# Kernel tuning notes

Measured on AMD Instinct MI355X. Metric: run time of the kernel, lower is better.

## Reference

```python
import jax, jax.numpy as jnp
import numpy as np

V, D, H, L, B, T = 32000, 1024, 1024, 4, 32, 128
PAD_ID = 0


def setup_inputs() -> dict:
    key = jax.random.key(0)
    ks = jax.random.split(key, 12)
    s = lambda fan: 1.0 / np.sqrt(fan)
    dec_input = jax.random.randint(ks[0], (B, T), 0, V)
    h0 = jax.random.normal(ks[1], (L, B, H), jnp.float32)
    c0 = jax.random.normal(ks[2], (L, B, H), jnp.float32)
    emb = jax.random.normal(ks[3], (V, D), jnp.float32) * 0.02
    emb = emb.at[PAD_ID].set(0.0)
    # all layers have input size H (layer0 input = embedding_dim = H)
    W_ih = jax.random.uniform(ks[4], (L, 4 * H, H), jnp.float32, -s(H), s(H))
    W_hh = jax.random.uniform(ks[5], (L, 4 * H, H), jnp.float32, -s(H), s(H))
    b_ih = jax.random.uniform(ks[6], (L, 4 * H), jnp.float32, -s(H), s(H))
    b_hh = jax.random.uniform(ks[7], (L, 4 * H), jnp.float32, -s(H), s(H))
    cls_W = jax.random.uniform(ks[8], (V, H), jnp.float32, -s(H), s(H))
    cls_b = jax.random.uniform(ks[9], (V,), jnp.float32, -s(H), s(H))
    return {"dec_input": dec_input, "h0": h0, "c0": c0, "emb": emb,
            "W_ih": W_ih, "W_hh": W_hh, "b_ih": b_ih, "b_hh": b_hh,
            "cls_W": cls_W, "cls_b": cls_b}


def _lstm_stack_step(carry, x_t, W_ih, W_hh, b_ih, b_hh):
    # carry: (h [L,B,H], c [L,B,H]); x_t: [B,H]
    h, c = carry
    inp = x_t
    hs, cs = [], []
    n_layers = W_ih.shape[0]
    for l in range(n_layers):
        gates = inp @ W_ih[l].T + h[l] @ W_hh[l].T + b_ih[l] + b_hh[l]
        i_g, f_g, g_g, o_g = jnp.split(gates, 4, axis=-1)
        c_new = jax.nn.sigmoid(f_g) * c[l] + jax.nn.sigmoid(i_g) * jnp.tanh(g_g)
        h_new = jax.nn.sigmoid(o_g) * jnp.tanh(c_new)
        inp = h_new + inp  # residual connection (dropout p=0)
        hs.append(h_new)
        cs.append(c_new)
    return (jnp.stack(hs, 0), jnp.stack(cs, 0)), inp


def reference(dec_input, h0, c0, emb, W_ih, W_hh, b_ih, b_hh, cls_W, cls_b):
    embedded = emb[dec_input]                 # [B,T,D]
    xs = jnp.swapaxes(embedded, 0, 1)         # [T,B,D]

    def step(carry, x_t):
        return _lstm_stack_step(carry, x_t, W_ih, W_hh, b_ih, b_hh)

    (hT, cT), outs = jax.lax.scan(step, (h0, c0), xs)  # outs: [T,B,H]
    outputs = jnp.swapaxes(outs, 0, 1)         # [B,T,H]
    logits = outputs @ cls_W.T + cls_b         # [B,T,V]
    return logits, (hT, cT)
```

## Files before the change

kernel.cpp:

```cpp
#include <hip/hip_runtime.h>
#include <stdint.h>

#define LAYERS 4
#define BATCH  32
#define SEQT   128
#define HID    1024
#define VOCAB  32000

typedef __attribute__((ext_vector_type(8))) short short8;
typedef __attribute__((ext_vector_type(8))) __bf16 bf16x8;
typedef __attribute__((ext_vector_type(4))) float floatx4;

#define CLS_OFF  0ul
#define X_OFF    65536000ul
#define RES_OFF  73924608ul
#define HB_OFF   107479040ul
#define CF_OFF   108003328ul
#define SYNC_OFF 108527616ul

#define LOGITS_N 131072000ul

__device__ __forceinline__ unsigned short f2bf(float f) {
  union { float f; unsigned u; } v; v.f = f;
  unsigned r = v.u + 0x7FFF + ((v.u >> 16) & 1);
  return (unsigned short)(r >> 16);
}
__device__ __forceinline__ float bf2f(unsigned short b) {
  union { unsigned u; float f; } v; v.u = ((unsigned)b) << 16;
  return v.f;
}
__device__ __forceinline__ floatx4 mfma16(short8 a, short8 b, floatx4 c) {
  return __builtin_amdgcn_mfma_f32_16x16x32_bf16(
      __builtin_bit_cast(bf16x8, a), __builtin_bit_cast(bf16x8, b), c, 0, 0, 0);
}
__device__ __forceinline__ short8 cvt8(float4 a, float4 b) {
  short8 r;
  r[0] = (short)f2bf(a.x); r[1] = (short)f2bf(a.y);
  r[2] = (short)f2bf(a.z); r[3] = (short)f2bf(a.w);
  r[4] = (short)f2bf(b.x); r[5] = (short)f2bf(b.y);
  r[6] = (short)f2bf(b.z); r[7] = (short)f2bf(b.w);
  return r;
}


__global__ void k_convert(const float* __restrict__ clsw, unsigned short* __restrict__ oC) {
  const long long NC4 = 8192000LL;
  for (long long i = (long long)blockIdx.x * blockDim.x + threadIdx.x; i < NC4;
       i += (long long)gridDim.x * blockDim.x) {
    float4 v = *(const float4*)(clsw + (i << 2));
    ushort4 o; o.x = f2bf(v.x); o.y = f2bf(v.y); o.z = f2bf(v.z); o.w = f2bf(v.w);
    *(ushort4*)(oC + (i << 2)) = o;
  }
}

__global__ void k_embed(const int* __restrict__ tok, const float* __restrict__ emb,
                        unsigned short* __restrict__ X) {
  const int bt = blockIdx.x;
  const int t = bt >> 5, b = bt & 31;
  const int v = tok[b * SEQT + t];
  const float4* src = (const float4*)(emb + (size_t)v * HID);
  ushort4* dst = (ushort4*)(X + (size_t)bt * HID);
  const int i = threadIdx.x;
  float4 f = src[i];
  ushort4 o; o.x = f2bf(f.x); o.y = f2bf(f.y); o.z = f2bf(f.z); o.w = f2bf(f.w);
  dst[i] = o;
}

__global__ void k_init(const float* __restrict__ h0, const float* __restrict__ c0,
                       unsigned short* __restrict__ HB, float* __restrict__ CF,
                       unsigned* __restrict__ sync) {
  const int i = blockIdx.x * blockDim.x + threadIdx.x;
  if (i < 4096) sync[i] = 0u;
  if (i < LAYERS * BATCH * HID) {
    HB[i] = f2bf(h0[i]);
    CF[i] = c0[i];
  }
}


__global__ __launch_bounds__(512, 2) void k_lstm(
    const float* __restrict__ Wih, const float* __restrict__ Whh,
    const float* __restrict__ bih, const float* __restrict__ bhh,
    const unsigned short* __restrict__ X, unsigned short* __restrict__ RES,
    unsigned short* __restrict__ HB, const float* __restrict__ CF,
    float* __restrict__ out, unsigned* __restrict__ syncp) {
  const int wg = blockIdx.x;
  const int l = wg >> 6;
  const int j0 = (wg & 63) << 4;
  const int tid = threadIdx.x;
  const int q = tid >> 6;
  const int lane = tid & 63;
  const int lo = lane & 15, hi = lane >> 4;
  const int u = tid & 15, b = tid >> 4;

  __shared__ float red[8][32][66];
  __shared__ unsigned mb;

  if (tid == 0) mb = 0u;

  const unsigned* fx = syncp + (((((l - 1) & 3) * 64) + lane) << 2);
  const unsigned* fh = syncp + (((l * 64) + lane) << 2);
  unsigned* fown = syncp + (((l * 64) + (wg & 63)) << 2);

  short8 wx[4][4], wh[4][4];
  {
    const size_t lb = (size_t)l * 4096;
#pragma unroll
    for (int ct = 0; ct < 4; ++ct) {
#pragma unroll
      for (int ks = 0; ks < 4; ++ks) {
        const size_t off = (lb + (size_t)(ct * 1024 + j0 + lo)) * HID
                         + (size_t)q * 128 + ks * 32 + hi * 8;
        float4 a0 = *(const float4*)(Wih + off);
        float4 a1 = *(const float4*)(Wih + off + 4);
        wx[ct][ks] = cvt8(a0, a1);
        float4 b0 = *(const float4*)(Whh + off);
        float4 b1 = *(const float4*)(Whh + off + 4);
        wh[ct][ks] = cvt8(b0, b1);
      }
    }
  }
  float bias_g[4];
#pragma unroll
  for (int g = 0; g < 4; ++g)
    bias_g[g] = bih[l * 4096 + g * 1024 + j0 + u] + bhh[l * 4096 + g * 1024 + j0 + u];
  float c_reg = CF[(size_t)l * (BATCH * HID) + (size_t)b * HID + j0 + u];

  __syncthreads();

  for (int t = 0; t < SEQT; ++t) {
    if (q == 0) {
      if (l > 0 || t > 0) {
        for (;;) {
          int ok = 1;
          if (l > 0)
            ok &= (__hip_atomic_load(fx, __ATOMIC_RELAXED, __HIP_MEMORY_SCOPE_AGENT)
                   >= (unsigned)(t + 1));
          if (t > 0)
            ok &= (__hip_atomic_load(fh, __ATOMIC_RELAXED, __HIP_MEMORY_SCOPE_AGENT)
                   >= (unsigned)t);
          if (__all(ok)) break;
          __builtin_amdgcn_s_sleep(1);
        }
      }
      __hip_atomic_store(&mb, (unsigned)(t + 1),
                         __ATOMIC_RELAXED, __HIP_MEMORY_SCOPE_WORKGROUP);
    } else {
      while (__hip_atomic_load(&mb, __ATOMIC_RELAXED, __HIP_MEMORY_SCOPE_WORKGROUP)
             < (unsigned)(t + 1))
        __builtin_amdgcn_s_sleep(1);
    }

    const unsigned short* xsrc = (l == 0)
        ? (X + (size_t)t * (BATCH * HID))
        : (RES + ((size_t)(l - 1) * SEQT + t) * (BATCH * HID));
    const unsigned short* hsrc = HB + ((size_t)(t & 1) * LAYERS + l) * (BATCH * HID);

    const unsigned short* px0 = xsrc + (size_t)lo * HID + q * 128 + hi * 8;
    const unsigned short* px1 = px0 + 16 * HID;
    const unsigned short* ph0 = hsrc + (size_t)lo * HID + q * 128 + hi * 8;
    const unsigned short* ph1 = ph0 + 16 * HID;
    const unsigned short* pxr = xsrc + (size_t)b * HID + j0 + u;

    short8 x0a, x0b, x0c, x0d, x1a, x1b, x1c, x1d;
    short8 h0a, h0b, h0c, h0d, h1a, h1b, h1c, h1d;
    unsigned xres;
    asm volatile(
      "global_load_dwordx4 %0,  %17, off sc0 sc1\n\t"
      "global_load_dwordx4 %1,  %17, off offset:64 sc0 sc1\n\t"
      "global_load_dwordx4 %2,  %17, off offset:128 sc0 sc1\n\t"
      "global_load_dwordx4 %3,  %17, off offset:192 sc0 sc1\n\t"
      "global_load_dwordx4 %4,  %18, off sc0 sc1\n\t"
      "global_load_dwordx4 %5,  %18, off offset:64 sc0 sc1\n\t"
      "global_load_dwordx4 %6,  %18, off offset:128 sc0 sc1\n\t"
      "global_load_dwordx4 %7,  %18, off offset:192 sc0 sc1\n\t"
      "global_load_dwordx4 %8,  %19, off sc0 sc1\n\t"
      "global_load_dwordx4 %9,  %19, off offset:64 sc0 sc1\n\t"
      "global_load_dwordx4 %10, %19, off offset:128 sc0 sc1\n\t"
      "global_load_dwordx4 %11, %19, off offset:192 sc0 sc1\n\t"
      "global_load_dwordx4 %12, %20, off sc0 sc1\n\t"
      "global_load_dwordx4 %13, %20, off offset:64 sc0 sc1\n\t"
      "global_load_dwordx4 %14, %20, off offset:128 sc0 sc1\n\t"
      "global_load_dwordx4 %15, %20, off offset:192 sc0 sc1\n\t"
      "global_load_ushort  %16, %21, off sc0 sc1\n\t"
      "s_waitcnt vmcnt(0)"
      : "=&v"(x0a), "=&v"(x0b), "=&v"(x0c), "=&v"(x0d),
        "=&v"(x1a), "=&v"(x1b), "=&v"(x1c), "=&v"(x1d),
        "=&v"(h0a), "=&v"(h0b), "=&v"(h0c), "=&v"(h0d),
        "=&v"(h1a), "=&v"(h1b), "=&v"(h1c), "=&v"(h1d),
        "=&v"(xres)
      : "v"(px0), "v"(px1), "v"(ph0), "v"(ph1), "v"(pxr)
      : "memory");

    floatx4 acc[4][2];
#pragma unroll
    for (int ct = 0; ct < 4; ++ct) { acc[ct][0] = {0,0,0,0}; acc[ct][1] = {0,0,0,0}; }
#pragma unroll
    for (int ct = 0; ct < 4; ++ct) {
      acc[ct][0] = mfma16(x0a, wx[ct][0], acc[ct][0]);
      acc[ct][1] = mfma16(x1a, wx[ct][0], acc[ct][1]);
      acc[ct][0] = mfma16(h0a, wh[ct][0], acc[ct][0]);
      acc[ct][1] = mfma16(h1a, wh[ct][0], acc[ct][1]);
      acc[ct][0] = mfma16(x0b, wx[ct][1], acc[ct][0]);
      acc[ct][1] = mfma16(x1b, wx[ct][1], acc[ct][1]);
      acc[ct][0] = mfma16(h0b, wh[ct][1], acc[ct][0]);
      acc[ct][1] = mfma16(h1b, wh[ct][1], acc[ct][1]);
      acc[ct][0] = mfma16(x0c, wx[ct][2], acc[ct][0]);
      acc[ct][1] = mfma16(x1c, wx[ct][2], acc[ct][1]);
      acc[ct][0] = mfma16(h0c, wh[ct][2], acc[ct][0]);
      acc[ct][1] = mfma16(h1c, wh[ct][2], acc[ct][1]);
      acc[ct][0] = mfma16(x0d, wx[ct][3], acc[ct][0]);
      acc[ct][1] = mfma16(x1d, wx[ct][3], acc[ct][1]);
      acc[ct][0] = mfma16(h0d, wh[ct][3], acc[ct][0]);
      acc[ct][1] = mfma16(h1d, wh[ct][3], acc[ct][1]);
    }

#pragma unroll
    for (int ct = 0; ct < 4; ++ct)
#pragma unroll
      for (int rt = 0; rt < 2; ++rt)
#pragma unroll
        for (int r = 0; r < 4; ++r)
          red[q][rt * 16 + hi * 4 + r][ct * 16 + lo] = acc[ct][rt][r];
    __syncthreads();

    float gacc[4] = {0.f, 0.f, 0.f, 0.f};
#pragma unroll
    for (int qq = 0; qq < 8; ++qq)
#pragma unroll
      for (int g = 0; g < 4; ++g)
        gacc[g] += red[qq][b][g * 16 + u];

    const float ig = gacc[0] + bias_g[0];
    const float fg = gacc[1] + bias_g[1];
    const float gg = gacc[2] + bias_g[2];
    const float og = gacc[3] + bias_g[3];
    const float si = 1.f / (1.f + __expf(-ig));
    const float sf = 1.f / (1.f + __expf(-fg));
    const float so = 1.f / (1.f + __expf(-og));
    const float tg = 1.f - 2.f / (__expf(2.f * gg) + 1.f);
    const float cn = sf * c_reg + si * tg;
    const float hn = so * (1.f - 2.f / (__expf(2.f * cn) + 1.f));
    c_reg = cn;

    const float xval = bf2f((unsigned short)xres);
    const unsigned hbf = f2bf(hn);
    const unsigned rbf = f2bf(hn + xval);
    const unsigned hpk = hbf | (((unsigned)__shfl_xor((int)hbf, 1)) << 16);
    const unsigned rpk = rbf | (((unsigned)__shfl_xor((int)rbf, 1)) << 16);

    unsigned short* HBw = HB + ((size_t)((t + 1) & 1) * LAYERS + l) * (BATCH * HID);
    unsigned short* RESw = RES + ((size_t)l * SEQT + t) * (BATCH * HID);
    const size_t hidx = (size_t)b * HID + j0 + u;
    if (!(tid & 1)) {
      __hip_atomic_store((unsigned*)(HBw + hidx), hpk,
                         __ATOMIC_RELAXED, __HIP_MEMORY_SCOPE_AGENT);
      __hip_atomic_store((unsigned*)(RESw + hidx), rpk,
                         __ATOMIC_RELAXED, __HIP_MEMORY_SCOPE_AGENT);
    }
    if (t == SEQT - 1) {
      out[LOGITS_N + (size_t)l * (BATCH * HID) + hidx] = hn;
      out[LOGITS_N + 131072ul + (size_t)l * (BATCH * HID) + hidx] = cn;
    }

    asm volatile("s_waitcnt vmcnt(0)" ::: "memory");
    __syncthreads();
    if (tid == 0)
      __hip_atomic_store(fown, (unsigned)(t + 1),
                         __ATOMIC_RELAXED, __HIP_MEMORY_SCOPE_AGENT);
  }
}


__global__ __launch_bounds__(256, 2) void k_cls(
    const unsigned short* __restrict__ A, const unsigned short* __restrict__ Bw,
    const float* __restrict__ bias, float* __restrict__ out) {
  __shared__ unsigned short lA[128 * 64];
  __shared__ unsigned short lB[128 * 64];
  const int ntile = blockIdx.x >> 5;
  const int mtile = blockIdx.x & 31;
  const int m0 = mtile << 7, n0 = ntile << 7;
  const int tid = threadIdx.x;
  const int w = tid >> 6, lane = tid & 63, lo = lane & 15, hi = lane >> 4;
  const int mw = (w >> 1) << 6, nw = (w & 1) << 6;

  floatx4 acc[4][4];
#pragma unroll
  for (int i = 0; i < 4; ++i)
#pragma unroll
    for (int j = 0; j < 4; ++j) acc[i][j] = {0.f, 0.f, 0.f, 0.f};

  for (int k0 = 0; k0 < HID; k0 += 64) {
#pragma unroll
    for (int qq = 0; qq < 4; ++qq) {
      const int e = qq * 256 + tid;
      const int row = e >> 3, c8 = e & 7;
      const int ps = row * 64 + ((c8 ^ (row & 7)) << 3);
      *(short8*)(lA + ps) = *(const short8*)(A  + (size_t)(m0 + row) * HID + k0 + (c8 << 3));
      *(short8*)(lB + ps) = *(const short8*)(Bw + (size_t)(n0 + row) * HID + k0 + (c8 << 3));
    }
    __syncthreads();
#pragma unroll
    for (int kk = 0; kk < 2; ++kk) {
      short8 af[4], bfr[4];
#pragma unroll
      for (int x = 0; x < 4; ++x) {
        const int ra = mw + x * 16 + lo;
        af[x]  = *(const short8*)(lA + ra * 64 + ((((kk << 2) + hi) ^ (ra & 7)) << 3));
        const int rb = nw + x * 16 + lo;
        bfr[x] = *(const short8*)(lB + rb * 64 + ((((kk << 2) + hi) ^ (rb & 7)) << 3));
      }
#pragma unroll
      for (int mi = 0; mi < 4; ++mi)
#pragma unroll
        for (int ni = 0; ni < 4; ++ni)
          acc[mi][ni] = mfma16(af[mi], bfr[ni], acc[mi][ni]);
    }
    __syncthreads();
  }

#pragma unroll
  for (int mi = 0; mi < 4; ++mi) {
#pragma unroll
    for (int ni = 0; ni < 4; ++ni) {
      const int v = n0 + nw + ni * 16 + lo;
      const float bv = bias[v];
#pragma unroll
      for (int r = 0; r < 4; ++r) {
        const int ra = m0 + mw + mi * 16 + hi * 4 + r;
        const int orow = (ra & 31) * SEQT + (ra >> 5);
        out[(size_t)orow * VOCAB + v] = acc[mi][ni][r] + bv;
      }
    }
  }
}


extern "C" void kernel_launch(void* const* d_in, const int* in_sizes, int n_in,
                              void* d_out, int out_size, void* d_ws, size_t ws_size,
                              hipStream_t stream) {
  (void)in_sizes; (void)n_in; (void)out_size; (void)ws_size;
  const int*   tok  = (const int*)d_in[0];
  const float* h0   = (const float*)d_in[1];
  const float* c0   = (const float*)d_in[2];
  const float* emb  = (const float*)d_in[3];
  const float* wih  = (const float*)d_in[4];
  const float* whh  = (const float*)d_in[5];
  const float* bih  = (const float*)d_in[6];
  const float* bhh  = (const float*)d_in[7];
  const float* clsw = (const float*)d_in[8];
  const float* clsb = (const float*)d_in[9];
  float* out = (float*)d_out;
  char* ws = (char*)d_ws;

  unsigned short* Cls = (unsigned short*)(ws + CLS_OFF);
  unsigned short* X   = (unsigned short*)(ws + X_OFF);
  unsigned short* RES = (unsigned short*)(ws + RES_OFF);
  unsigned short* HB  = (unsigned short*)(ws + HB_OFF);
  float*          CF  = (float*)(ws + CF_OFF);
  unsigned*       SY  = (unsigned*)(ws + SYNC_OFF);

  hipLaunchKernelGGL(k_convert, dim3(2048), dim3(256), 0, stream, clsw, Cls);
  hipLaunchKernelGGL(k_embed,   dim3(SEQT * BATCH), dim3(256), 0, stream, tok, emb, X);
  hipLaunchKernelGGL(k_init,    dim3(512), dim3(256), 0, stream, h0, c0, HB, CF, SY);

  {
    const float* a0 = wih; const float* a1 = whh; const float* a2 = bih; const float* a3 = bhh;
    const unsigned short* a4 = X; unsigned short* a5 = RES; unsigned short* a6 = HB;
    const float* a7 = CF; float* a8 = out; unsigned* a9 = SY;
    void* kargs[] = {&a0, &a1, &a2, &a3, &a4, &a5, &a6, &a7, &a8, &a9};
    hipLaunchCooperativeKernel((void*)k_lstm, dim3(256), dim3(512), kargs, 0, stream);
  }

  hipLaunchKernelGGL(k_cls, dim3(250 * 32), dim3(256), 0, stream,
                     RES + (size_t)3 * SEQT * BATCH * HID, Cls, clsb, out);
}
```

Baseline: 1.423 ms.

## Split LSTM step wait into input and hidden phases, overlap input-projection MFMAs

Each LSTM workgroup now waits only on the previous layer's flag before loading x and running the input-projection MFMAs, then waits on its own layer's hidden-state flag before loading h and finishing the gate accumulation. The hidden-state buffer grows from double-buffered to one slot per timestep, which lets the loads drop the sc0/sc1 cache-bypass bits. Workgroups are also remapped so that blocks of different layers interleave across the grid. The goal is to take the W_ih x work off the recurrent critical path, at the cost of a larger workspace and a second spin-wait per step.

```diff
diff --git a/kernel.cpp b/kernel.cpp
--- a/kernel.cpp
+++ b/kernel.cpp
@@ -14,11 +14,12 @@
 #define CLS_OFF  0ul
 #define X_OFF    65536000ul
 #define RES_OFF  73924608ul
-#define HB_OFF   107479040ul
-#define CF_OFF   108003328ul
-#define SYNC_OFF 108527616ul
+#define HBT_OFF  107479040ul
+#define CF_OFF   141295616ul
+#define SYNC_OFF 141819904ul
 
 #define LOGITS_N 131072000ul
+#define BH (BATCH * HID)
 
 __device__ __forceinline__ unsigned short f2bf(float f) {
   union { float f; unsigned u; } v; v.f = f;
@@ -67,12 +68,12 @@
 }
 
 __global__ void k_init(const float* __restrict__ h0, const float* __restrict__ c0,
-                       unsigned short* __restrict__ HB, float* __restrict__ CF,
+                       unsigned short* __restrict__ HBT, float* __restrict__ CF,
                        unsigned* __restrict__ sync) {
   const int i = blockIdx.x * blockDim.x + threadIdx.x;
   if (i < 4096) sync[i] = 0u;
   if (i < LAYERS * BATCH * HID) {
-    HB[i] = f2bf(h0[i]);
+    HBT[i] = f2bf(h0[i]);
     CF[i] = c0[i];
   }
 }
@@ -82,11 +83,12 @@
     const float* __restrict__ Wih, const float* __restrict__ Whh,
     const float* __restrict__ bih, const float* __restrict__ bhh,
     const unsigned short* __restrict__ X, unsigned short* __restrict__ RES,
-    unsigned short* __restrict__ HB, const float* __restrict__ CF,
+    unsigned short* __restrict__ HBT, const float* __restrict__ CF,
     float* __restrict__ out, unsigned* __restrict__ syncp) {
-  const int wg = blockIdx.x;
-  const int l = wg >> 6;
-  const int j0 = (wg & 63) << 4;
+  const int p = blockIdx.x;
+  const int l = (p & 7) >> 1;
+  const int jj = ((p >> 3) << 1) | (p & 1);
+  const int j0 = jj << 4;
   const int tid = threadIdx.x;
   const int q = tid >> 6;
   const int lane = tid & 63;
@@ -94,13 +96,15 @@
   const int u = tid & 15, b = tid >> 4;
 
   __shared__ float red[8][32][66];
-  __shared__ unsigned mb;
-
-  if (tid == 0) mb = 0u;
-
-  const unsigned* fx = syncp + (((((l - 1) & 3) * 64) + lane) << 2);
-  const unsigned* fh = syncp + (((l * 64) + lane) << 2);
-  unsigned* fown = syncp + (((l * 64) + (wg & 63)) << 2);
+  __shared__ unsigned mbx, mbh;
+
+  if (tid == 0) { mbx = 0u; mbh = 0u; }
+
+  (void)__hip_atomic_load(syncp + 2048, __ATOMIC_ACQUIRE, __HIP_MEMORY_SCOPE_AGENT);
+
+  const unsigned* fx = syncp + (((l - 1) & 3) * 64 + lane) * 4;
+  const unsigned* fh = syncp + (l * 64 + lane) * 4;
+  unsigned* fown = syncp + (l * 64 + jj) * 4;
 
   short8 wx[4][4], wh[4][4];
   {
@@ -124,72 +128,52 @@
 #pragma unroll
   for (int g = 0; g < 4; ++g)
     bias_g[g] = bih[l * 4096 + g * 1024 + j0 + u] + bhh[l * 4096 + g * 1024 + j0 + u];
-  float c_reg = CF[(size_t)l * (BATCH * HID) + (size_t)b * HID + j0 + u];
+  float c_reg = CF[(size_t)l * BH + (size_t)b * HID + j0 + u];
 
   __syncthreads();
 
   for (int t = 0; t < SEQT; ++t) {
     if (q == 0) {
-      if (l > 0 || t > 0) {
+      if (l > 0) {
         for (;;) {
-          int ok = 1;
-          if (l > 0)
-            ok &= (__hip_atomic_load(fx, __ATOMIC_RELAXED, __HIP_MEMORY_SCOPE_AGENT)
-                   >= (unsigned)(t + 1));
-          if (t > 0)
-            ok &= (__hip_atomic_load(fh, __ATOMIC_RELAXED, __HIP_MEMORY_SCOPE_AGENT)
-                   >= (unsigned)t);
+          int ok = (__hip_atomic_load(fx, __ATOMIC_RELAXED, __HIP_MEMORY_SCOPE_AGENT)
+                    >= (unsigned)(t + 1));
           if (__all(ok)) break;
           __builtin_amdgcn_s_sleep(1);
         }
       }
-      __hip_atomic_store(&mb, (unsigned)(t + 1),
+      __hip_atomic_store(&mbx, (unsigned)(t + 1),
                          __ATOMIC_RELAXED, __HIP_MEMORY_SCOPE_WORKGROUP);
     } else {
-      while (__hip_atomic_load(&mb, __ATOMIC_RELAXED, __HIP_MEMORY_SCOPE_WORKGROUP)
+      while (__hip_atomic_load(&mbx, __ATOMIC_RELAXED, __HIP_MEMORY_SCOPE_WORKGROUP)
              < (unsigned)(t + 1))
         __builtin_amdgcn_s_sleep(1);
     }
 
     const unsigned short* xsrc = (l == 0)
-        ? (X + (size_t)t * (BATCH * HID))
-        : (RES + ((size_t)(l - 1) * SEQT + t) * (BATCH * HID));
-    const unsigned short* hsrc = HB + ((size_t)(t & 1) * LAYERS + l) * (BATCH * HID);
+        ? (X + (size_t)t * BH)
+        : (RES + ((size_t)(l - 1) * SEQT + t) * BH);
 
     const unsigned short* px0 = xsrc + (size_t)lo * HID + q * 128 + hi * 8;
     const unsigned short* px1 = px0 + 16 * HID;
-    const unsigned short* ph0 = hsrc + (size_t)lo * HID + q * 128 + hi * 8;
-    const unsigned short* ph1 = ph0 + 16 * HID;
     const unsigned short* pxr = xsrc + (size_t)b * HID + j0 + u;
 
     short8 x0a, x0b, x0c, x0d, x1a, x1b, x1c, x1d;
-    short8 h0a, h0b, h0c, h0d, h1a, h1b, h1c, h1d;
     unsigned xres;
     asm volatile(
-      "global_load_dwordx4 %0,  %17, off sc0 sc1\n\t"
-      "global_load_dwordx4 %1,  %17, off offset:64 sc0 sc1\n\t"
-      "global_load_dwordx4 %2,  %17, off offset:128 sc0 sc1\n\t"
-      "global_load_dwordx4 %3,  %17, off offset:192 sc0 sc1\n\t"
-      "global_load_dwordx4 %4,  %18, off sc0 sc1\n\t"
-      "global_load_dwordx4 %5,  %18, off offset:64 sc0 sc1\n\t"
-      "global_load_dwordx4 %6,  %18, off offset:128 sc0 sc1\n\t"
-      "global_load_dwordx4 %7,  %18, off offset:192 sc0 sc1\n\t"
-      "global_load_dwordx4 %8,  %19, off sc0 sc1\n\t"
-      "global_load_dwordx4 %9,  %19, off offset:64 sc0 sc1\n\t"
-      "global_load_dwordx4 %10, %19, off offset:128 sc0 sc1\n\t"
-      "global_load_dwordx4 %11, %19, off offset:192 sc0 sc1\n\t"
-      "global_load_dwordx4 %12, %20, off sc0 sc1\n\t"
-      "global_load_dwordx4 %13, %20, off offset:64 sc0 sc1\n\t"
-      "global_load_dwordx4 %14, %20, off offset:128 sc0 sc1\n\t"
-      "global_load_dwordx4 %15, %20, off offset:192 sc0 sc1\n\t"
-      "global_load_ushort  %16, %21, off sc0 sc1\n\t"
+      "global_load_dwordx4 %0, %9,  off\n\t"
+      "global_load_dwordx4 %1, %9,  off offset:64\n\t"
+      "global_load_dwordx4 %2, %9,  off offset:128\n\t"
+      "global_load_dwordx4 %3, %9,  off offset:192\n\t"
+      "global_load_dwordx4 %4, %10, off\n\t"
+      "global_load_dwordx4 %5, %10, off offset:64\n\t"
+      "global_load_dwordx4 %6, %10, off offset:128\n\t"
+      "global_load_dwordx4 %7, %10, off offset:192\n\t"
+      "global_load_ushort  %8, %11, off\n\t"
       "s_waitcnt vmcnt(0)"
       : "=&v"(x0a), "=&v"(x0b), "=&v"(x0c), "=&v"(x0d),
-        "=&v"(x1a), "=&v"(x1b), "=&v"(x1c), "=&v"(x1d),
-        "=&v"(h0a), "=&v"(h0b), "=&v"(h0c), "=&v"(h0d),
-        "=&v"(h1a), "=&v"(h1b), "=&v"(h1c), "=&v"(h1d),
-        "=&v"(xres)
-      : "v"(px0), "v"(px1), "v"(ph0), "v"(ph1), "v"(pxr)
+        "=&v"(x1a), "=&v"(x1b), "=&v"(x1c), "=&v"(x1d), "=&v"(xres)
+      : "v"(px0), "v"(px1), "v"(pxr)
       : "memory");
 
     floatx4 acc[4][2];
@@ -199,18 +183,59 @@
     for (int ct = 0; ct < 4; ++ct) {
       acc[ct][0] = mfma16(x0a, wx[ct][0], acc[ct][0]);
       acc[ct][1] = mfma16(x1a, wx[ct][0], acc[ct][1]);
+      acc[ct][0] = mfma16(x0b, wx[ct][1], acc[ct][0]);
+      acc[ct][1] = mfma16(x1b, wx[ct][1], acc[ct][1]);
+      acc[ct][0] = mfma16(x0c, wx[ct][2], acc[ct][0]);
+      acc[ct][1] = mfma16(x1c, wx[ct][2], acc[ct][1]);
+      acc[ct][0] = mfma16(x0d, wx[ct][3], acc[ct][0]);
+      acc[ct][1] = mfma16(x1d, wx[ct][3], acc[ct][1]);
+    }
+
+    if (q == 0) {
+      if (t > 0) {
+        for (;;) {
+          int ok = (__hip_atomic_load(fh, __ATOMIC_RELAXED, __HIP_MEMORY_SCOPE_AGENT)
+                    >= (unsigned)t);
+          if (__all(ok)) break;
+          __builtin_amdgcn_s_sleep(1);
+        }
+      }
+      __hip_atomic_store(&mbh, (unsigned)(t + 1),
+                         __ATOMIC_RELAXED, __HIP_MEMORY_SCOPE_WORKGROUP);
+    } else {
+      while (__hip_atomic_load(&mbh, __ATOMIC_RELAXED, __HIP_MEMORY_SCOPE_WORKGROUP)
+             < (unsigned)(t + 1))
+        __builtin_amdgcn_s_sleep(1);
+    }
+
+    const unsigned short* hsrc = HBT + ((size_t)t * LAYERS + l) * BH;
+    const unsigned short* ph0 = hsrc + (size_t)lo * HID + q * 128 + hi * 8;
+    const unsigned short* ph1 = ph0 + 16 * HID;
+
+    short8 h0a, h0b, h0c, h0d, h1a, h1b, h1c, h1d;
+    asm volatile(
+      "global_load_dwordx4 %0, %8, off\n\t"
+      "global_load_dwordx4 %1, %8, off offset:64\n\t"
+      "global_load_dwordx4 %2, %8, off offset:128\n\t"
+      "global_load_dwordx4 %3, %8, off offset:192\n\t"
+      "global_load_dwordx4 %4, %9, off\n\t"
+      "global_load_dwordx4 %5, %9, off offset:64\n\t"
+      "global_load_dwordx4 %6, %9, off offset:128\n\t"
+      "global_load_dwordx4 %7, %9, off offset:192\n\t"
+      "s_waitcnt vmcnt(0)"
+      : "=&v"(h0a), "=&v"(h0b), "=&v"(h0c), "=&v"(h0d),
+        "=&v"(h1a), "=&v"(h1b), "=&v"(h1c), "=&v"(h1d)
+      : "v"(ph0), "v"(ph1)
+      : "memory");
+
+#pragma unroll
+    for (int ct = 0; ct < 4; ++ct) {
       acc[ct][0] = mfma16(h0a, wh[ct][0], acc[ct][0]);
       acc[ct][1] = mfma16(h1a, wh[ct][0], acc[ct][1]);
-      acc[ct][0] = mfma16(x0b, wx[ct][1], acc[ct][0]);
-      acc[ct][1] = mfma16(x1b, wx[ct][1], acc[ct][1]);
       acc[ct][0] = mfma16(h0b, wh[ct][1], acc[ct][0]);
       acc[ct][1] = mfma16(h1b, wh[ct][1], acc[ct][1]);
-      acc[ct][0] = mfma16(x0c, wx[ct][2], acc[ct][0]);
-      acc[ct][1] = mfma16(x1c, wx[ct][2], acc[ct][1]);
       acc[ct][0] = mfma16(h0c, wh[ct][2], acc[ct][0]);
       acc[ct][1] = mfma16(h1c, wh[ct][2], acc[ct][1]);
-      acc[ct][0] = mfma16(x0d, wx[ct][3], acc[ct][0]);
-      acc[ct][1] = mfma16(x1d, wx[ct][3], acc[ct][1]);
       acc[ct][0] = mfma16(h0d, wh[ct][3], acc[ct][0]);
       acc[ct][1] = mfma16(h1d, wh[ct][3], acc[ct][1]);
     }
@@ -249,8 +274,8 @@
     const unsigned hpk = hbf | (((unsigned)__shfl_xor((int)hbf, 1)) << 16);
     const unsigned rpk = rbf | (((unsigned)__shfl_xor((int)rbf, 1)) << 16);
 
-    unsigned short* HBw = HB + ((size_t)((t + 1) & 1) * LAYERS + l) * (BATCH * HID);
-    unsigned short* RESw = RES + ((size_t)l * SEQT + t) * (BATCH * HID);
+    unsigned short* HBw = HBT + ((size_t)(t + 1) * LAYERS + l) * BH;
+    unsigned short* RESw = RES + ((size_t)l * SEQT + t) * BH;
     const size_t hidx = (size_t)b * HID + j0 + u;
     if (!(tid & 1)) {
       __hip_atomic_store((unsigned*)(HBw + hidx), hpk,
@@ -259,8 +284,8 @@
                          __ATOMIC_RELAXED, __HIP_MEMORY_SCOPE_AGENT);
     }
     if (t == SEQT - 1) {
-      out[LOGITS_N + (size_t)l * (BATCH * HID) + hidx] = hn;
-      out[LOGITS_N + 131072ul + (size_t)l * (BATCH * HID) + hidx] = cn;
+      out[LOGITS_N + (size_t)l * BH + hidx] = hn;
+      out[LOGITS_N + 131072ul + (size_t)l * BH + hidx] = cn;
     }
 
     asm volatile("s_waitcnt vmcnt(0)" ::: "memory");
@@ -356,17 +381,17 @@
   unsigned short* Cls = (unsigned short*)(ws + CLS_OFF);
   unsigned short* X   = (unsigned short*)(ws + X_OFF);
   unsigned short* RES = (unsigned short*)(ws + RES_OFF);
-  unsigned short* HB  = (unsigned short*)(ws + HB_OFF);
+  unsigned short* HBT = (unsigned short*)(ws + HBT_OFF);
   float*          CF  = (float*)(ws + CF_OFF);
   unsigned*       SY  = (unsigned*)(ws + SYNC_OFF);
 
   hipLaunchKernelGGL(k_convert, dim3(2048), dim3(256), 0, stream, clsw, Cls);
   hipLaunchKernelGGL(k_embed,   dim3(SEQT * BATCH), dim3(256), 0, stream, tok, emb, X);
-  hipLaunchKernelGGL(k_init,    dim3(512), dim3(256), 0, stream, h0, c0, HB, CF, SY);
+  hipLaunchKernelGGL(k_init,    dim3(512), dim3(256), 0, stream, h0, c0, HBT, CF, SY);
 
   {
     const float* a0 = wih; const float* a1 = whh; const float* a2 = bih; const float* a3 = bhh;
-    const unsigned short* a4 = X; unsigned short* a5 = RES; unsigned short* a6 = HB;
+    const unsigned short* a4 = X; unsigned short* a5 = RES; unsigned short* a6 = HBT;
     const float* a7 = CF; float* a8 = out; unsigned* a9 = SY;
     void* kargs[] = {&a0, &a1, &a2, &a3, &a4, &a5, &a6, &a7, &a8, &a9};
     hipLaunchCooperativeKernel((void*)k_lstm, dim3(256), dim3(512), kargs, 0, stream);
```

New measurement: 1.288 ms. 1.1x faster.
